# Optimization experiments

Hardware: AMD Instinct MI355X
Metric: run time of the kernel (lower is better)

## Reference

```python
import jax, jax.numpy as jnp
import numpy as np

N_COLS = 4096
N_ROWS = 4096
H = 64          # args.hidden1
S = 2           # per-edge supp feature count (cv_supp/vc_supp dim 0)
S_VO = 2        # vo_supp feature dim
S_CO = 2        # co_supp feature dim
EDGE_DENSITY = 0.03


def setup_inputs() -> dict:
    key = jax.random.key(0)
    ks = jax.random.split(key, 20)
    col_hidden = jax.random.normal(ks[0], (N_COLS, H), jnp.float32)
    row_hidden = jax.random.normal(ks[1], (N_ROWS, H), jnp.float32)
    obj_hidden = jax.random.normal(ks[2], (1, H), jnp.float32)
    # sparse bipartite adjacency encoded in supp[0] != 0 (as in the TF code)
    mask = jax.random.bernoulli(ks[3], EDGE_DENSITY, (N_ROWS, N_COLS))
    cv_supp = jax.random.normal(ks[4], (S, N_ROWS, N_COLS), jnp.float32) * mask[None]
    vc_supp = jnp.transpose(cv_supp, (0, 2, 1))  # [S, ncols, nrows]
    vo_supp = jax.random.normal(ks[5], (N_COLS, S_VO), jnp.float32)
    co_supp = jax.random.normal(ks[6], (N_ROWS, S_CO), jnp.float32)
    w = 0.05
    W_vo = jax.random.normal(ks[7], (2 * H, H), jnp.float32) * w
    W_oc = jax.random.normal(ks[8], (2 * H, H), jnp.float32) * w
    W_vc = jax.random.normal(ks[9], (2 * H, H), jnp.float32) * w
    W_co = jax.random.normal(ks[10], (2 * H, H), jnp.float32) * w
    W_ov = jax.random.normal(ks[11], (2 * H, H), jnp.float32) * w
    W_cv = jax.random.normal(ks[12], (2 * H, H), jnp.float32) * w
    # attention scorer nets: Dense(concat_dim -> 1) + sigmoid
    w_attn_vo = jax.random.normal(ks[13], (2 * H + S_VO, 1), jnp.float32) * 0.1
    b_attn_vo = jnp.zeros((), jnp.float32)
    w_attn_co = jax.random.normal(ks[14], (2 * H + S_CO, 1), jnp.float32) * 0.1
    b_attn_co = jnp.zeros((), jnp.float32)
    # pairwise attn nets decomposed into [col | supp | row] weight slices
    w_cv_col = jax.random.normal(ks[15], (H,), jnp.float32) * 0.1
    w_cv_supp = jax.random.normal(ks[16], (S,), jnp.float32) * 0.1
    w_cv_row = jax.random.normal(ks[17], (H,), jnp.float32) * 0.1
    b_cv = jnp.zeros((), jnp.float32)
    w_vc_row = jax.random.normal(ks[18], (H,), jnp.float32) * 0.1
    w_vc_supp = jax.random.normal(ks[19], (S,), jnp.float32) * 0.1
    w_vc_col = jax.random.normal(jax.random.fold_in(key, 99), (H,), jnp.float32) * 0.1
    b_vc = jnp.zeros((), jnp.float32)
    return dict(col_hidden=col_hidden, row_hidden=row_hidden, obj_hidden=obj_hidden,
                cv_supp=cv_supp, vc_supp=vc_supp, vo_supp=vo_supp, co_supp=co_supp,
                W_vo=W_vo, W_oc=W_oc, W_vc=W_vc, W_co=W_co, W_ov=W_ov, W_cv=W_cv,
                w_attn_vo=w_attn_vo, b_attn_vo=b_attn_vo,
                w_attn_co=w_attn_co, b_attn_co=b_attn_co,
                w_cv_col=w_cv_col, w_cv_supp=w_cv_supp, w_cv_row=w_cv_row, b_cv=b_cv,
                w_vc_row=w_vc_row, w_vc_supp=w_vc_supp, w_vc_col=w_vc_col, b_vc=b_vc)


def _forward(col_hidden, row_hidden, obj_hidden, cv_supp, vc_supp, vo_supp, co_supp,
             W_vo, W_oc, W_vc, W_co, W_ov, W_cv,
             w_attn_vo, b_attn_vo, w_attn_co, b_attn_co,
             w_cv_col, w_cv_supp, w_cv_row, b_cv,
             w_vc_row, w_vc_supp, w_vc_col, b_vc):
    act = jax.nn.relu
    ncols, nrows = col_hidden.shape[0], row_hidden.shape[0]
    # ---- v -> o: attend over all columns, update obj node ----
    vo_in = jnp.concatenate([col_hidden, vo_supp,
                             jnp.broadcast_to(obj_hidden, (ncols, H))], axis=1)
    a_vo = jax.nn.sigmoid(vo_in @ w_attn_vo + b_attn_vo)          # [ncols, 1]
    v_o_out = a_vo.T @ col_hidden                                  # [1, H]
    obj = act(jnp.concatenate([obj_hidden, v_o_out], axis=1) @ W_vo)
    # ---- v -> c: per-row ragged neighbor attention, vectorized via masked pairwise scores ----
    nbr_cv = cv_supp[0] != 0                                       # [nrows, ncols]
    logits_cv = ((row_hidden @ w_cv_row)[:, None]
                 + (col_hidden @ w_cv_col)[None, :]
                 + jnp.einsum('snc,s->nc', cv_supp, w_cv_supp) + b_cv)
    score_cv = jnp.where(nbr_cv, jax.nn.sigmoid(logits_cv), 0.0)   # [nrows, ncols]
    v_out = score_cv @ col_hidden                                  # [nrows, H]
    o_c_out = act(jnp.concatenate([jnp.broadcast_to(obj, (nrows, H)), row_hidden], axis=1) @ W_oc)
    row_next = act(jnp.concatenate([o_c_out, v_out], axis=1) @ W_vc)
    # ---- c -> o ----
    co_in = jnp.concatenate([row_next, co_supp,
                             jnp.broadcast_to(obj, (nrows, H))], axis=1)
    a_co = jax.nn.sigmoid(co_in @ w_attn_co + b_attn_co)           # [nrows, 1]
    c_o_out = a_co.T @ row_next                                    # [1, H]
    obj = act(jnp.concatenate([obj, c_o_out], axis=1) @ W_co)
    # ---- c -> v ----
    nbr_vc = vc_supp[0] != 0                                       # [ncols, nrows]
    logits_vc = ((col_hidden @ w_vc_col)[:, None]
                 + (row_next @ w_vc_row)[None, :]
                 + jnp.einsum('scn,s->cn', vc_supp, w_vc_supp) + b_vc)
    score_vc = jnp.where(nbr_vc, jax.nn.sigmoid(logits_vc), 0.0)   # [ncols, nrows]
    c_out = score_vc @ row_next                                    # [ncols, H]
    o_v_out = act(jnp.concatenate([jnp.broadcast_to(obj, (ncols, H)), col_hidden], axis=1) @ W_ov)
    col_next = act(jnp.concatenate([o_v_out, c_out], axis=1) @ W_cv)
    return col_next, row_next, obj


def reference(col_hidden, row_hidden, obj_hidden, cv_supp, vc_supp, vo_supp, co_supp,
              W_vo, W_oc, W_vc, W_co, W_ov, W_cv,
              w_attn_vo, b_attn_vo, w_attn_co, b_attn_co,
              w_cv_col, w_cv_supp, w_cv_row, b_cv,
              w_vc_row, w_vc_supp, w_vc_col, b_vc):
    col_next, row_next, obj = _forward(
        col_hidden, row_hidden, obj_hidden, cv_supp, vc_supp, vo_supp, co_supp,
        W_vo, W_oc, W_vc, W_co, W_ov, W_cv,
        w_attn_vo, b_attn_vo, w_attn_co, b_attn_co,
        w_cv_col, w_cv_supp, w_cv_row, b_cv,
        w_vc_row, w_vc_supp, w_vc_col, b_vc)
    # original layer also passes the supp tensors through unchanged
    return (col_next, row_next, obj, cv_supp, vc_supp, vo_supp, co_supp)
```

## Files before the change

### kernel.cpp

```cpp
#include <hip/hip_runtime.h>
#include <math.h>

typedef float f4 __attribute__((ext_vector_type(4)));

#define PLANE (4096*4096)

#define OUT_COL 0
#define OUT_ROW 262144
#define OUT_OBJ 524288
#define OUT_CV  524352
#define OUT_VC  34078784
#define OUT_VO  67633216
#define OUT_CO  67641408

#define WS_VO_P 0
#define WS_CO_P 1024
#define WS_OBJ1 2048
#define WS_RDCV 2112
#define WS_CDCV 6208
#define WS_RDVC 10304
#define WS_CDVC 14400
#define WS_PART 18496

__device__ __forceinline__ float sigf(float x) {
    return 1.0f / (1.0f + __expf(-x));
}

__device__ __forceinline__ void attn_body(
    int blk, int t, const float* __restrict__ X, const float* __restrict__ supp,
    const float* __restrict__ obj, const float* __restrict__ wat,
    const float* __restrict__ bat, float* __restrict__ accP,
    const float* __restrict__ wextra, float* __restrict__ dextra,
    float* sA, float* sAcc)
{
    const int i = blk * 256 + t;
    float od = 0.f;
    for (int h = 0; h < 64; ++h) od += obj[h] * wat[66 + h];
    float x = bat[0] + od + supp[i*2] * wat[64] + supp[i*2+1] * wat[65];
    const f4* Xr = (const f4*)(X + i*64);
    f4 xd = 0.f, dd = 0.f;
    #pragma unroll
    for (int q = 0; q < 16; ++q) {
        f4 xv = Xr[q];
        xd += xv * ((const f4*)wat)[q];
        if (wextra) dd += xv * ((const f4*)wextra)[q];
    }
    x += xd.x + xd.y + xd.z + xd.w;
    if (dextra) dextra[i] = dd.x + dd.y + dd.z + dd.w;
    sA[t] = sigf(x);
    if (t < 64) sAcc[t] = 0.f;
    __syncthreads();
    const int w = t >> 6, h = t & 63;
    const int base = blk * 256 + w * 64;
    float partial = 0.f;
    for (int j = 0; j < 64; ++j)
        partial += sA[w*64 + j] * X[(base + j)*64 + h];
    atomicAdd(&sAcc[h], partial);
    __syncthreads();
    if (t < 64) accP[blk*64 + t] = sAcc[t];
}

__global__ __launch_bounds__(256) void k_front(
    const float* __restrict__ col_hidden, const float* __restrict__ row_hidden,
    const float* __restrict__ w_cv_col, const float* __restrict__ w_vc_col,
    const float* __restrict__ w_cv_row,
    float* __restrict__ cdcv, float* __restrict__ cdvc, float* __restrict__ rdcv,
    const float* __restrict__ vo_supp, const float* __restrict__ co_supp,
    float* __restrict__ out_vo, float* __restrict__ out_co,
    const float* __restrict__ obj_hidden, const float* __restrict__ w_attn_vo,
    const float* __restrict__ b_attn_vo, float* __restrict__ voP)
{
    __shared__ float sA[256];
    __shared__ float sAcc[64];
    const int t = threadIdx.x;
    if (blockIdx.x < 3072) {
        const int gw = blockIdx.x * 4 + (t >> 6);
        const int lane = t & 63;
        const int which = gw >> 12;
        const int row = gw & 4095;
        const float* x; const float* w; float* dst;
        if (which == 0)      { x = col_hidden; w = w_cv_col; dst = cdcv; }
        else if (which == 1) { x = col_hidden; w = w_vc_col; dst = cdvc; }
        else                 { x = row_hidden; w = w_cv_row; dst = rdcv; }
        float v = x[row * 64 + lane] * w[lane];
        #pragma unroll
        for (int off = 32; off; off >>= 1) v += __shfl_down(v, off, 64);
        if (lane == 0) dst[row] = v;
        return;
    }
    if (blockIdx.x < 3088) {
        const int idx = (blockIdx.x - 3072) * 256 + t;
        if (idx < 2048) ((f4*)out_vo)[idx] = ((const f4*)vo_supp)[idx];
        else            ((f4*)out_co)[idx - 2048] = ((const f4*)co_supp)[idx - 2048];
        return;
    }
    attn_body(blockIdx.x - 3088, t, col_hidden, vo_supp, obj_hidden,
              w_attn_vo, b_attn_vo, voP, nullptr, nullptr, sA, sAcc);
}

__global__ __launch_bounds__(256) void k_attn(
    const float* __restrict__ X, const float* __restrict__ supp,
    const float* __restrict__ obj, const float* __restrict__ wat,
    const float* __restrict__ bat, float* __restrict__ accP,
    const float* __restrict__ wextra, float* __restrict__ dextra)
{
    __shared__ float sA[256];
    __shared__ float sAcc[64];
    attn_body(blockIdx.x, threadIdx.x, X, supp, obj, wat, bat, accP,
              wextra, dextra, sA, sAcc);
}

__global__ __launch_bounds__(256, 4) void k_big(
    const float* __restrict__ supp0, const float* __restrict__ supp1,
    const float* __restrict__ Bm,
    const float* __restrict__ rdot, const float* __restrict__ cdot,
    const float* __restrict__ wsup, const float* __restrict__ bias,
    float* __restrict__ part, float* __restrict__ pass0, float* __restrict__ pass1,
    const float* __restrict__ objL, const float* __restrict__ objRp,
    const float* __restrict__ Wobj, float* __restrict__ objDst)
{
    __shared__ __align__(16) float sS[64][68];
    __shared__ __align__(16) float sB[64][64];
    const int t = threadIdx.x;

    if (blockIdx.x == 1024) {
        float* rsum = &sS[0][0];
        if (t < 64) {
            float r = 0.f;
            for (int b = 0; b < 16; ++b) r += objRp[b*64 + t];
            rsum[t] = r;
        }
        __syncthreads();
        if (t < 64) {
            float acc = 0.f;
            for (int k = 0; k < 64; ++k) acc += objL[k] * Wobj[k*64 + t];
            for (int k = 0; k < 64; ++k) acc += rsum[k] * Wobj[(64+k)*64 + t];
            objDst[t] = fmaxf(acc, 0.f);
        }
        return;
    }

    const int bi = blockIdx.x & 63;
    const int bj = blockIdx.x >> 6;
    const int i0 = bi * 64;
    const int jl4 = (t & 15) * 4;
    const int ilb = t >> 4;
    const float w0 = wsup[0], w1 = wsup[1], bv = bias[0];

    f4 acc0 = 0.f, acc1 = 0.f, acc2 = 0.f, acc3 = 0.f;

    for (int tile = 0; tile < 4; ++tile) {
        const int jt = bj * 256 + tile * 64;
        {
            const f4* src = (const f4*)(Bm + (size_t)jt * 64);
            f4* dstp = (f4*)&sB[0][0];
            dstp[t]       = src[t];
            dstp[t + 256] = src[t + 256];
            dstp[t + 512] = src[t + 512];
            dstp[t + 768] = src[t + 768];
        }
        const f4 cd = *(const f4*)(cdot + jt + jl4);
        #pragma unroll
        for (int k = 0; k < 4; ++k) {
            const int il = ilb + 16 * k;
            const size_t idx = (size_t)(i0 + il) * 4096 + jt + jl4;
            f4 a0 = *(const f4*)(supp0 + idx);
            f4 a1 = *(const f4*)(supp1 + idx);
            __builtin_nontemporal_store(a0, (f4*)(pass0 + idx));
            __builtin_nontemporal_store(a1, (f4*)(pass1 + idx));
            const float rd = rdot[i0 + il];
            f4 lg = rd + cd + w0 * a0 + w1 * a1 + bv;
            f4 s;
            s.x = (a0.x != 0.f) ? sigf(lg.x) : 0.f;
            s.y = (a0.y != 0.f) ? sigf(lg.y) : 0.f;
            s.z = (a0.z != 0.f) ? sigf(lg.z) : 0.f;
            s.w = (a0.w != 0.f) ? sigf(lg.w) : 0.f;
            *(f4*)&sS[il][jl4] = s;
        }
        __syncthreads();
        const int h0 = jl4;
        #pragma unroll
        for (int jj = 0; jj < 64; jj += 4) {
            f4 b0 = *(const f4*)&sB[jj + 0][h0];
            f4 b1 = *(const f4*)&sB[jj + 1][h0];
            f4 b2 = *(const f4*)&sB[jj + 2][h0];
            f4 b3 = *(const f4*)&sB[jj + 3][h0];
            { f4 s = *(const f4*)&sS[ilb*4 + 0][jj]; acc0 += s.x*b0 + s.y*b1 + s.z*b2 + s.w*b3; }
            { f4 s = *(const f4*)&sS[ilb*4 + 1][jj]; acc1 += s.x*b0 + s.y*b1 + s.z*b2 + s.w*b3; }
            { f4 s = *(const f4*)&sS[ilb*4 + 2][jj]; acc2 += s.x*b0 + s.y*b1 + s.z*b2 + s.w*b3; }
            { f4 s = *(const f4*)&sS[ilb*4 + 3][jj]; acc3 += s.x*b0 + s.y*b1 + s.z*b2 + s.w*b3; }
        }
        __syncthreads();
    }
    float* pb = part + (size_t)bj * 262144 + (size_t)i0 * 64;
    *(f4*)(pb + (ilb*4 + 0)*64 + jl4) = acc0;
    *(f4*)(pb + (ilb*4 + 1)*64 + jl4) = acc1;
    *(f4*)(pb + (ilb*4 + 2)*64 + jl4) = acc2;
    *(f4*)(pb + (ilb*4 + 3)*64 + jl4) = acc3;
}

__global__ __launch_bounds__(256) void k_mlp2(
    const float* __restrict__ objx, const float* __restrict__ base,
    const float* __restrict__ W1, const float* __restrict__ part,
    const float* __restrict__ W2, float* __restrict__ dst)
{
    __shared__ float mid[4][64];
    __shared__ float accs[4][64];
    const int t = threadIdx.x, w = t >> 6, h = t & 63;
    const int n = blockIdx.x * 4 + w;
    float v = 0.f;
    #pragma unroll
    for (int j = 0; j < 16; ++j) v += part[(size_t)j * 262144 + n*64 + h];
    accs[w][h] = v;
    float m = 0.f;
    for (int k = 0; k < 64; ++k) m += objx[k] * W1[k*64 + h];
    for (int k = 0; k < 64; ++k) m += base[n*64 + k] * W1[(64+k)*64 + h];
    mid[w][h] = fmaxf(m, 0.f);
    __syncthreads();
    float o = 0.f;
    for (int k = 0; k < 64; ++k) o += mid[w][k] * W2[k*64 + h];
    for (int k = 0; k < 64; ++k) o += accs[w][k] * W2[(64+k)*64 + h];
    dst[n*64 + h] = fmaxf(o, 0.f);
}

extern "C" void kernel_launch(void* const* d_in, const int* in_sizes, int n_in,
                              void* d_out, int out_size, void* d_ws, size_t ws_size,
                              hipStream_t stream)
{
    const float* col_hidden = (const float*)d_in[0];
    const float* row_hidden = (const float*)d_in[1];
    const float* obj_hidden = (const float*)d_in[2];
    const float* cv_supp    = (const float*)d_in[3];
    const float* vc_supp    = (const float*)d_in[4];
    const float* vo_supp    = (const float*)d_in[5];
    const float* co_supp    = (const float*)d_in[6];
    const float* W_vo       = (const float*)d_in[7];
    const float* W_oc       = (const float*)d_in[8];
    const float* W_vc       = (const float*)d_in[9];
    const float* W_co       = (const float*)d_in[10];
    const float* W_ov       = (const float*)d_in[11];
    const float* W_cv       = (const float*)d_in[12];
    const float* w_attn_vo  = (const float*)d_in[13];
    const float* b_attn_vo  = (const float*)d_in[14];
    const float* w_attn_co  = (const float*)d_in[15];
    const float* b_attn_co  = (const float*)d_in[16];
    const float* w_cv_col   = (const float*)d_in[17];
    const float* w_cv_supp  = (const float*)d_in[18];
    const float* w_cv_row   = (const float*)d_in[19];
    const float* b_cv       = (const float*)d_in[20];
    const float* w_vc_row   = (const float*)d_in[21];
    const float* w_vc_supp  = (const float*)d_in[22];
    const float* w_vc_col   = (const float*)d_in[23];
    const float* b_vc       = (const float*)d_in[24];

    float* out = (float*)d_out;
    float* ws  = (float*)d_ws;

    k_front<<<3104, 256, 0, stream>>>(col_hidden, row_hidden, w_cv_col, w_vc_col, w_cv_row,
                                      ws + WS_CDCV, ws + WS_CDVC, ws + WS_RDCV,
                                      vo_supp, co_supp, out + OUT_VO, out + OUT_CO,
                                      obj_hidden, w_attn_vo, b_attn_vo, ws + WS_VO_P);
    k_big<<<1025, 256, 0, stream>>>(cv_supp, cv_supp + PLANE, col_hidden,
                                    ws + WS_RDCV, ws + WS_CDCV, w_cv_supp, b_cv,
                                    ws + WS_PART, out + OUT_CV, out + OUT_CV + PLANE,
                                    obj_hidden, ws + WS_VO_P, W_vo, ws + WS_OBJ1);
    k_mlp2<<<1024, 256, 0, stream>>>(ws + WS_OBJ1, row_hidden, W_oc, ws + WS_PART, W_vc,
                                     out + OUT_ROW);
    k_attn<<<16, 256, 0, stream>>>(out + OUT_ROW, co_supp, ws + WS_OBJ1, w_attn_co, b_attn_co,
                                   ws + WS_CO_P, w_vc_row, ws + WS_RDVC);
    k_big<<<1025, 256, 0, stream>>>(vc_supp, vc_supp + PLANE, out + OUT_ROW,
                                    ws + WS_CDVC, ws + WS_RDVC, w_vc_supp, b_vc,
                                    ws + WS_PART, out + OUT_VC, out + OUT_VC + PLANE,
                                    ws + WS_OBJ1, ws + WS_CO_P, W_co, out + OUT_OBJ);
    k_mlp2<<<1024, 256, 0, stream>>>(out + OUT_OBJ, col_hidden, W_ov, ws + WS_PART, W_cv,
                                     out + OUT_COL);
}
```

Measured before the change: 573.1 us.

## Split score computation from matmul and use bf16 MFMA for aggregation

Splits the fused score-plus-matmul kernel into a streaming kernel that writes bf16 attention scores to a workspace and a separate GEMM kernel using bf16 MFMA instructions against a bf16 transposed hidden matrix. The transposed bf16 operands are built inside the existing front and attention kernels, and split-K drops from 16 to 8 partials. The aim is to replace slow fp32 LDS-based FMA accumulation with matrix cores. The cost is an extra round trip of the score plane through memory, plus reduced precision in the aggregation.

```diff
diff --git a/kernel.cpp b/kernel.cpp
--- a/kernel.cpp
+++ b/kernel.cpp
@@ -1,7 +1,10 @@
 #include <hip/hip_runtime.h>
 #include <math.h>
 
-typedef float f4 __attribute__((ext_vector_type(4)));
+typedef float f4  __attribute__((ext_vector_type(4)));
+typedef short s8v __attribute__((ext_vector_type(8)));
+typedef unsigned short u16;
+typedef u16 us4 __attribute__((ext_vector_type(4)));
 
 #define PLANE (4096*4096)
 
@@ -13,17 +16,48 @@
 #define OUT_VO  67633216
 #define OUT_CO  67641408
 
-#define WS_VO_P 0
-#define WS_CO_P 1024
-#define WS_OBJ1 2048
-#define WS_RDCV 2112
-#define WS_CDCV 6208
-#define WS_RDVC 10304
-#define WS_CDVC 14400
-#define WS_PART 18496
+#define WS_VO_P  0
+#define WS_CO_P  1024
+#define WS_OBJ1  2048
+#define WS_RDCV  2112
+#define WS_CDCV  6208
+#define WS_RDVC  10304
+#define WS_CDVC  14400
+#define WS_GPART 18496
+#define WS_SC    2115648
+#define WS_BT1   10504256
+#define WS_BT2   10635328
 
 __device__ __forceinline__ float sigf(float x) {
     return 1.0f / (1.0f + __expf(-x));
+}
+__device__ __forceinline__ u16 f2bf(float x) {
+    unsigned u = __float_as_uint(x);
+    return (u16)((u + 0x7FFFu + ((u >> 16) & 1u)) >> 16);
+}
+
+__device__ __forceinline__ void transpose_tile(int k0, int t,
+    const float* __restrict__ X, u16* __restrict__ BT, float* lds )
+{
+    #pragma unroll
+    for (int it = 0; it < 4; ++it) {
+        const int idx = it * 256 + t;
+        const int r = idx >> 4, c4 = (idx & 15) * 4;
+        f4 v = *(const f4*)(X + (size_t)(k0 + r) * 64 + c4);
+        *(f4*)(lds + r * 72 + c4) = v;
+    }
+    __syncthreads();
+    #pragma unroll
+    for (int it = 0; it < 4; ++it) {
+        const int idx = it * 256 + t;
+        const int h = idx >> 4, q = (idx & 15) * 4;
+        us4 o;
+        o.x = f2bf(lds[(q + 0) * 72 + h]);
+        o.y = f2bf(lds[(q + 1) * 72 + h]);
+        o.z = f2bf(lds[(q + 2) * 72 + h]);
+        o.w = f2bf(lds[(q + 3) * 72 + h]);
+        *(us4*)(BT + (size_t)h * 4096 + k0 + q) = o;
+    }
 }
 
 __device__ __forceinline__ void attn_body(
@@ -68,10 +102,12 @@
     const float* __restrict__ vo_supp, const float* __restrict__ co_supp,
     float* __restrict__ out_vo, float* __restrict__ out_co,
     const float* __restrict__ obj_hidden, const float* __restrict__ w_attn_vo,
-    const float* __restrict__ b_attn_vo, float* __restrict__ voP)
+    const float* __restrict__ b_attn_vo, float* __restrict__ voP,
+    u16* __restrict__ BT1)
 {
     __shared__ float sA[256];
     __shared__ float sAcc[64];
+    __shared__ float tr[64*72];
     const int t = threadIdx.x;
     if (blockIdx.x < 3072) {
         const int gw = blockIdx.x * 4 + (t >> 6);
@@ -94,37 +130,70 @@
         else            ((f4*)out_co)[idx - 2048] = ((const f4*)co_supp)[idx - 2048];
         return;
     }
-    attn_body(blockIdx.x - 3088, t, col_hidden, vo_supp, obj_hidden,
-              w_attn_vo, b_attn_vo, voP, nullptr, nullptr, sA, sAcc);
+    if (blockIdx.x < 3104) {
+        attn_body(blockIdx.x - 3088, t, col_hidden, vo_supp, obj_hidden,
+                  w_attn_vo, b_attn_vo, voP, nullptr, nullptr, sA, sAcc);
+        return;
+    }
+    transpose_tile((blockIdx.x - 3104) * 64, t, col_hidden, BT1, tr);
 }
 
 __global__ __launch_bounds__(256) void k_attn(
     const float* __restrict__ X, const float* __restrict__ supp,
     const float* __restrict__ obj, const float* __restrict__ wat,
     const float* __restrict__ bat, float* __restrict__ accP,
-    const float* __restrict__ wextra, float* __restrict__ dextra)
+    const float* __restrict__ wextra, float* __restrict__ dextra,
+    u16* __restrict__ BT2)
 {
     __shared__ float sA[256];
     __shared__ float sAcc[64];
-    attn_body(blockIdx.x, threadIdx.x, X, supp, obj, wat, bat, accP,
-              wextra, dextra, sA, sAcc);
-}
-
-__global__ __launch_bounds__(256, 4) void k_big(
+    __shared__ float tr[64*72];
+    if (blockIdx.x < 16) {
+        attn_body(blockIdx.x, threadIdx.x, X, supp, obj, wat, bat, accP,
+                  wextra, dextra, sA, sAcc);
+        return;
+    }
+    transpose_tile((blockIdx.x - 16) * 64, threadIdx.x, X, BT2, tr);
+}
+
+__global__ __launch_bounds__(256, 8) void k_stream(
     const float* __restrict__ supp0, const float* __restrict__ supp1,
-    const float* __restrict__ Bm,
-    const float* __restrict__ rdot, const float* __restrict__ cdot,
+    const float* __restrict__ perrow, const float* __restrict__ percol,
     const float* __restrict__ wsup, const float* __restrict__ bias,
-    float* __restrict__ part, float* __restrict__ pass0, float* __restrict__ pass1,
+    float* __restrict__ pass0, float* __restrict__ pass1,
+    u16* __restrict__ score)
+{
+    const float w0 = wsup[0], w1 = wsup[1], bv = bias[0];
+    const int N4 = PLANE / 4;
+    const int stride = gridDim.x * 256;
+    for (int idx = blockIdx.x * 256 + threadIdx.x; idx < N4; idx += stride) {
+        const int row = idx >> 10;
+        const int j0  = (idx & 1023) * 4;
+        f4 a0 = ((const f4*)supp0)[idx];
+        f4 a1 = ((const f4*)supp1)[idx];
+        __builtin_nontemporal_store(a0, (f4*)pass0 + idx);
+        __builtin_nontemporal_store(a1, (f4*)pass1 + idx);
+        const float rd = perrow[row];
+        f4 cd = *(const f4*)(percol + j0);
+        f4 lg = rd + cd + w0 * a0 + w1 * a1 + bv;
+        us4 o;
+        o.x = (a0.x != 0.f) ? f2bf(sigf(lg.x)) : (u16)0;
+        o.y = (a0.y != 0.f) ? f2bf(sigf(lg.y)) : (u16)0;
+        o.z = (a0.z != 0.f) ? f2bf(sigf(lg.z)) : (u16)0;
+        o.w = (a0.w != 0.f) ? f2bf(sigf(lg.w)) : (u16)0;
+        ((us4*)score)[idx] = o;
+    }
+}
+
+__global__ __launch_bounds__(256, 4) void k_gemm(
+    const u16* __restrict__ sc, const u16* __restrict__ BT,
+    float* __restrict__ part,
     const float* __restrict__ objL, const float* __restrict__ objRp,
     const float* __restrict__ Wobj, float* __restrict__ objDst)
 {
-    __shared__ __align__(16) float sS[64][68];
-    __shared__ __align__(16) float sB[64][64];
+    __shared__ float rsum[64];
     const int t = threadIdx.x;
-
-    if (blockIdx.x == 1024) {
-        float* rsum = &sS[0][0];
+    if (blockIdx.x == 512) {
         if (t < 64) {
             float r = 0.f;
             for (int b = 0; b < 16; ++b) r += objRp[b*64 + t];
@@ -139,64 +208,37 @@
         }
         return;
     }
-
-    const int bi = blockIdx.x & 63;
-    const int bj = blockIdx.x >> 6;
-    const int i0 = bi * 64;
-    const int jl4 = (t & 15) * 4;
-    const int ilb = t >> 4;
-    const float w0 = wsup[0], w1 = wsup[1], bv = bias[0];
+    const int mblk = blockIdx.x >> 3;
+    const int ks   = blockIdx.x & 7;
+    const int wv   = t >> 6, lane = t & 63;
+    const int i0   = mblk * 64 + wv * 16;
+    const int m    = lane & 15, quad = lane >> 4;
+    const int k0   = ks * 512;
 
     f4 acc0 = 0.f, acc1 = 0.f, acc2 = 0.f, acc3 = 0.f;
-
-    for (int tile = 0; tile < 4; ++tile) {
-        const int jt = bj * 256 + tile * 64;
-        {
-            const f4* src = (const f4*)(Bm + (size_t)jt * 64);
-            f4* dstp = (f4*)&sB[0][0];
-            dstp[t]       = src[t];
-            dstp[t + 256] = src[t + 256];
-            dstp[t + 512] = src[t + 512];
-            dstp[t + 768] = src[t + 768];
-        }
-        const f4 cd = *(const f4*)(cdot + jt + jl4);
-        #pragma unroll
-        for (int k = 0; k < 4; ++k) {
-            const int il = ilb + 16 * k;
-            const size_t idx = (size_t)(i0 + il) * 4096 + jt + jl4;
-            f4 a0 = *(const f4*)(supp0 + idx);
-            f4 a1 = *(const f4*)(supp1 + idx);
-            __builtin_nontemporal_store(a0, (f4*)(pass0 + idx));
-            __builtin_nontemporal_store(a1, (f4*)(pass1 + idx));
-            const float rd = rdot[i0 + il];
-            f4 lg = rd + cd + w0 * a0 + w1 * a1 + bv;
-            f4 s;
-            s.x = (a0.x != 0.f) ? sigf(lg.x) : 0.f;
-            s.y = (a0.y != 0.f) ? sigf(lg.y) : 0.f;
-            s.z = (a0.z != 0.f) ? sigf(lg.z) : 0.f;
-            s.w = (a0.w != 0.f) ? sigf(lg.w) : 0.f;
-            *(f4*)&sS[il][jl4] = s;
-        }
-        __syncthreads();
-        const int h0 = jl4;
-        #pragma unroll
-        for (int jj = 0; jj < 64; jj += 4) {
-            f4 b0 = *(const f4*)&sB[jj + 0][h0];
-            f4 b1 = *(const f4*)&sB[jj + 1][h0];
-            f4 b2 = *(const f4*)&sB[jj + 2][h0];
-            f4 b3 = *(const f4*)&sB[jj + 3][h0];
-            { f4 s = *(const f4*)&sS[ilb*4 + 0][jj]; acc0 += s.x*b0 + s.y*b1 + s.z*b2 + s.w*b3; }
-            { f4 s = *(const f4*)&sS[ilb*4 + 1][jj]; acc1 += s.x*b0 + s.y*b1 + s.z*b2 + s.w*b3; }
-            { f4 s = *(const f4*)&sS[ilb*4 + 2][jj]; acc2 += s.x*b0 + s.y*b1 + s.z*b2 + s.w*b3; }
-            { f4 s = *(const f4*)&sS[ilb*4 + 3][jj]; acc3 += s.x*b0 + s.y*b1 + s.z*b2 + s.w*b3; }
-        }
-        __syncthreads();
-    }
-    float* pb = part + (size_t)bj * 262144 + (size_t)i0 * 64;
-    *(f4*)(pb + (ilb*4 + 0)*64 + jl4) = acc0;
-    *(f4*)(pb + (ilb*4 + 1)*64 + jl4) = acc1;
-    *(f4*)(pb + (ilb*4 + 2)*64 + jl4) = acc2;
-    *(f4*)(pb + (ilb*4 + 3)*64 + jl4) = acc3;
+    const u16* ap  = sc + (size_t)(i0 + m) * 4096 + k0 + quad * 8;
+    const u16* bp  = BT + (size_t)m * 4096 + k0 + quad * 8;
+    #pragma unroll 4
+    for (int kc = 0; kc < 512; kc += 32) {
+        s8v a  = *(const s8v*)(ap + kc);
+        s8v b0 = *(const s8v*)(bp + kc);
+        s8v b1 = *(const s8v*)(bp + 16 * 4096 + kc);
+        s8v b2 = *(const s8v*)(bp + 32 * 4096 + kc);
+        s8v b3 = *(const s8v*)(bp + 48 * 4096 + kc);
+        acc0 = __builtin_amdgcn_mfma_f32_16x16x32_bf16(a, b0, acc0, 0, 0, 0);
+        acc1 = __builtin_amdgcn_mfma_f32_16x16x32_bf16(a, b1, acc1, 0, 0, 0);
+        acc2 = __builtin_amdgcn_mfma_f32_16x16x32_bf16(a, b2, acc2, 0, 0, 0);
+        acc3 = __builtin_amdgcn_mfma_f32_16x16x32_bf16(a, b3, acc3, 0, 0, 0);
+    }
+    float* pb = part + (size_t)ks * 262144;
+    #pragma unroll
+    for (int r = 0; r < 4; ++r) {
+        const size_t ro = (size_t)(i0 + quad * 4 + r) * 64 + m;
+        pb[ro +  0] = acc0[r];
+        pb[ro + 16] = acc1[r];
+        pb[ro + 32] = acc2[r];
+        pb[ro + 48] = acc3[r];
+    }
 }
 
 __global__ __launch_bounds__(256) void k_mlp2(
@@ -210,7 +252,7 @@
     const int n = blockIdx.x * 4 + w;
     float v = 0.f;
     #pragma unroll
-    for (int j = 0; j < 16; ++j) v += part[(size_t)j * 262144 + n*64 + h];
+    for (int j = 0; j < 8; ++j) v += part[(size_t)j * 262144 + n*64 + h];
     accs[w][h] = v;
     float m = 0.f;
     for (int k = 0; k < 64; ++k) m += objx[k] * W1[k*64 + h];
@@ -255,23 +297,28 @@
 
     float* out = (float*)d_out;
     float* ws  = (float*)d_ws;
-
-    k_front<<<3104, 256, 0, stream>>>(col_hidden, row_hidden, w_cv_col, w_vc_col, w_cv_row,
+    u16* SC  = (u16*)(ws + WS_SC);
+    u16* BT1 = (u16*)(ws + WS_BT1);
+    u16* BT2 = (u16*)(ws + WS_BT2);
+
+    k_front<<<3168, 256, 0, stream>>>(col_hidden, row_hidden, w_cv_col, w_vc_col, w_cv_row,
                                       ws + WS_CDCV, ws + WS_CDVC, ws + WS_RDCV,
                                       vo_supp, co_supp, out + OUT_VO, out + OUT_CO,
-                                      obj_hidden, w_attn_vo, b_attn_vo, ws + WS_VO_P);
-    k_big<<<1025, 256, 0, stream>>>(cv_supp, cv_supp + PLANE, col_hidden,
-                                    ws + WS_RDCV, ws + WS_CDCV, w_cv_supp, b_cv,
-                                    ws + WS_PART, out + OUT_CV, out + OUT_CV + PLANE,
+                                      obj_hidden, w_attn_vo, b_attn_vo, ws + WS_VO_P, BT1);
+    k_stream<<<4096, 256, 0, stream>>>(cv_supp, cv_supp + PLANE,
+                                       ws + WS_RDCV, ws + WS_CDCV, w_cv_supp, b_cv,
+                                       out + OUT_CV, out + OUT_CV + PLANE, SC);
+    k_gemm<<<513, 256, 0, stream>>>(SC, BT1, ws + WS_GPART,
                                     obj_hidden, ws + WS_VO_P, W_vo, ws + WS_OBJ1);
-    k_mlp2<<<1024, 256, 0, stream>>>(ws + WS_OBJ1, row_hidden, W_oc, ws + WS_PART, W_vc,
+    k_mlp2<<<1024, 256, 0, stream>>>(ws + WS_OBJ1, row_hidden, W_oc, ws + WS_GPART, W_vc,
                                      out + OUT_ROW);
-    k_attn<<<16, 256, 0, stream>>>(out + OUT_ROW, co_supp, ws + WS_OBJ1, w_attn_co, b_attn_co,
-                                   ws + WS_CO_P, w_vc_row, ws + WS_RDVC);
-    k_big<<<1025, 256, 0, stream>>>(vc_supp, vc_supp + PLANE, out + OUT_ROW,
-                                    ws + WS_CDVC, ws + WS_RDVC, w_vc_supp, b_vc,
-                                    ws + WS_PART, out + OUT_VC, out + OUT_VC + PLANE,
+    k_attn<<<80, 256, 0, stream>>>(out + OUT_ROW, co_supp, ws + WS_OBJ1, w_attn_co,
+                                   b_attn_co, ws + WS_CO_P, w_vc_row, ws + WS_RDVC, BT2);
+    k_stream<<<4096, 256, 0, stream>>>(vc_supp, vc_supp + PLANE,
+                                       ws + WS_CDVC, ws + WS_RDVC, w_vc_supp, b_vc,
+                                       out + OUT_VC, out + OUT_VC + PLANE, SC);
+    k_gemm<<<513, 256, 0, stream>>>(SC, BT2, ws + WS_GPART,
                                     ws + WS_OBJ1, ws + WS_CO_P, W_co, out + OUT_OBJ);
-    k_mlp2<<<1024, 256, 0, stream>>>(out + OUT_OBJ, col_hidden, W_ov, ws + WS_PART, W_cv,
+    k_mlp2<<<1024, 256, 0, stream>>>(out + OUT_OBJ, col_hidden, W_ov, ws + WS_GPART, W_cv,
                                      out + OUT_COL);
 }
```

Measured after the change: 588.5 us. +2.7%, slower.
